# Optimization experiments

Hardware: AMD Instinct MI355X
Metric: run time of the kernel (lower is better)

The kernel has to match this reference:

```python
import jax, jax.numpy as jnp
import numpy as np
from jax import lax

CS = 64  # c_star


def _conv(x, w, pad, dil=1, groups=1):
    return lax.conv_general_dilated(
        x, w, (1, 1), ((pad[0], pad[0]), (pad[1], pad[1])),
        rhs_dilation=(dil, dil), dimension_numbers=('NCHW', 'OIHW', 'NCHW'),
        feature_group_count=groups)


def _bn(x, p, eps=1e-5):
    # p: [4, C] = (gamma, beta, running_mean, running_var), eval-mode batchnorm
    g, b, m, v = p
    s = g * lax.rsqrt(v + eps)
    return x * s[None, :, None, None] + (b - m * s)[None, :, None, None]


def _grid_sample(im, grid):
    # bilinear, padding_mode='zeros', align_corners=True
    # im: [B,C,H,W], grid: [B,H,W,2] with (x, y) in [-1, 1]
    B, C, H, W = im.shape
    gx = (grid[..., 0] + 1.0) * 0.5 * (W - 1)
    gy = (grid[..., 1] + 1.0) * 0.5 * (H - 1)
    x0 = jnp.floor(gx)
    y0 = jnp.floor(gy)
    wx = gx - x0
    wy = gy - y0

    def corner(ix, iy, w):
        valid = (ix >= 0) & (ix <= W - 1) & (iy >= 0) & (iy <= H - 1)
        ixc = jnp.clip(ix, 0, W - 1).astype(jnp.int32)
        iyc = jnp.clip(iy, 0, H - 1).astype(jnp.int32)
        vals = jax.vmap(lambda a, yy, xx: a[:, yy, xx])(im, iyc, ixc)  # [B,C,H,W]
        return vals * (w * valid)[:, None]

    return (corner(x0, y0, (1 - wx) * (1 - wy)) + corner(x0 + 1, y0, wx * (1 - wy))
            + corner(x0, y0 + 1, (1 - wx) * wy) + corner(x0 + 1, y0 + 1, wx * wy))


def _forward(x, w_reduce, bn_reduce, dcn_off_w, dcn_off_b, dcn_dw_w, dcn_pw_w, bn_dcn,
             w_d2, bn_d2, w_d3, bn_d3, w_asym1, bn_asym1, w_asym2, bn_asym2,
             ctx_weight, bn_star, eca_w, sp_w, blend_weight, w_expand, bn_expand):
    silu = jax.nn.silu
    h = silu(_bn(_conv(x, w_reduce, (0, 0)), bn_reduce))
    hs, hb = h[:, :CS], h[:, CS:]
    B, _, H, W = hs.shape
    # --- LightweightDCNv2 ---
    om = _conv(hs, dcn_off_w, (1, 1)) + dcn_off_b[None, :, None, None]
    off_y, off_x = om[:, 0], om[:, 1]
    mask = jax.nn.sigmoid(om[:, 2:3])
    gy, gx = jnp.meshgrid(jnp.linspace(-1.0, 1.0, H), jnp.linspace(-1.0, 1.0, W), indexing='ij')
    grid = jnp.stack([gx[None] + off_x * (2.0 / W), gy[None] + off_y * (2.0 / H)], axis=-1)
    xd = _grid_sample(hs, grid) * mask
    dcn = silu(_bn(_conv(_conv(xd, dcn_dw_w, (1, 1), groups=CS), dcn_pw_w, (0, 0)), bn_dcn))
    # --- context branches (depthwise dilated + asymmetric) ---
    d2 = silu(_bn(_conv(hs, w_d2, (2, 2), dil=2, groups=CS), bn_d2))
    d3 = silu(_bn(_conv(hs, w_d3, (3, 3), dil=3, groups=CS), bn_d3))
    a1 = silu(_bn(_conv(hs, w_asym1, (0, 3), groups=CS), bn_asym1))
    asym = silu(_bn(_conv(a1, w_asym2, (3, 0), groups=CS), bn_asym2))
    wv = jax.nn.softmax(ctx_weight)
    ctx = wv[0] * d2 + wv[1] * d3 + wv[2] * asym
    star = _bn(dcn * ctx, bn_star)
    # --- DualAttentionGate ---
    ych = star.mean((2, 3))[:, None, :]  # [B,1,C]
    ych = lax.conv_general_dilated(ych, eca_w, (1,), ((2, 2),),
                                   dimension_numbers=('NCH', 'OIH', 'NCH'))
    ych = jax.nn.sigmoid(ych).reshape(B, CS, 1, 1)
    star = star * ych
    sp = jnp.concatenate([star.mean(1, keepdims=True), star.max(1, keepdims=True)], axis=1)
    star = star * jax.nn.sigmoid(_conv(sp, sp_w, (3, 3)))
    # --- blend + shuffle + expand + residual ---
    alpha = jax.nn.sigmoid(blend_weight)
    out = jnp.concatenate([star * alpha, hb * (1.0 - alpha)], axis=1)
    c = out.shape[1]
    out = out.reshape(B, 2, c // 2, H, W).transpose(0, 2, 1, 3, 4).reshape(B, c, H, W)
    out = silu(_bn(_conv(out, w_expand, (0, 0)), bn_expand))
    return out + x


def setup_inputs() -> dict:
    ks = iter(jax.random.split(jax.random.key(0), 64))

    def nrm(shape, s=0.05):
        return jax.random.normal(next(ks), shape, jnp.float32) * s

    def bnp(C):
        return jnp.stack([1.0 + nrm((C,), 0.1), nrm((C,), 0.1), nrm((C,), 0.1),
                          0.5 + jax.random.uniform(next(ks), (C,), jnp.float32)])

    C1, C_, CSTAR = 256, 128, 64
    return dict(
        x=jax.random.normal(next(ks), (16, C1, 80, 80), jnp.float32),
        w_reduce=nrm((C_, C1, 1, 1)),
        bn_reduce=bnp(C_),
        dcn_off_w=nrm((3, CSTAR, 3, 3), 0.01),
        dcn_off_b=nrm((3,), 0.01),
        dcn_dw_w=nrm((CSTAR, 1, 3, 3), 0.2),
        dcn_pw_w=nrm((CSTAR, CSTAR, 1, 1), 0.1),
        bn_dcn=bnp(CSTAR),
        w_d2=nrm((CSTAR, 1, 3, 3), 0.2),
        bn_d2=bnp(CSTAR),
        w_d3=nrm((CSTAR, 1, 3, 3), 0.2),
        bn_d3=bnp(CSTAR),
        w_asym1=nrm((CSTAR, 1, 1, 7), 0.2),
        bn_asym1=bnp(CSTAR),
        w_asym2=nrm((CSTAR, 1, 7, 1), 0.2),
        bn_asym2=bnp(CSTAR),
        ctx_weight=jnp.ones(3, jnp.float32) / 3.0,
        bn_star=bnp(CSTAR),
        eca_w=nrm((1, 1, 5), 0.3),
        sp_w=nrm((1, 2, 7, 7), 0.1),
        blend_weight=jnp.asarray(0.5, jnp.float32),
        w_expand=nrm((C1, C_, 1, 1)),
        bn_expand=bnp(C1),
    )


def reference(x, w_reduce, bn_reduce, dcn_off_w, dcn_off_b, dcn_dw_w, dcn_pw_w, bn_dcn,
              w_d2, bn_d2, w_d3, bn_d3, w_asym1, bn_asym1, w_asym2, bn_asym2,
              ctx_weight, bn_star, eca_w, sp_w, blend_weight, w_expand, bn_expand):
    return _forward(x, w_reduce, bn_reduce, dcn_off_w, dcn_off_b, dcn_dw_w, dcn_pw_w, bn_dcn,
                    w_d2, bn_d2, w_d3, bn_d3, w_asym1, bn_asym1, w_asym2, bn_asym2,
                    ctx_weight, bn_star, eca_w, sp_w, blend_weight, w_expand, bn_expand)
```

## Files before the change

### kernel.cpp

```cpp
#include <hip/hip_runtime.h>

#define HH 80
#define WW 80
#define HWN 6400
#define BN 16

typedef unsigned short ushortT;
typedef __attribute__((ext_vector_type(8))) short short8;
typedef __attribute__((ext_vector_type(4))) float f32x4;

static constexpr size_t BIGN = (size_t)BN * 64 * HWN;

__device__ __forceinline__ float sigf(float v)  { return 1.f / (1.f + __expf(-v)); }
__device__ __forceinline__ float siluf(float v) { return v * sigf(v); }
__device__ __forceinline__ float bnap(float v, const float* __restrict__ bn, int c, int C) {
  float s = bn[c] * rsqrtf(bn[3 * C + c] + 1e-5f);
  return v * s + (bn[C + c] - bn[2 * C + c] * s);
}
__device__ __forceinline__ ushortT f2bf(float f) {
  unsigned u = __float_as_uint(f);
  return (ushortT)((u + 0x7FFFu + ((u >> 16) & 1u)) >> 16);
}
__device__ __forceinline__ void gl_lds16(const void* g, void* l) {
  __builtin_amdgcn_global_load_lds(
      (const __attribute__((address_space(1))) unsigned int*)g,
      (__attribute__((address_space(3))) unsigned int*)l, 16, 0, 0);
}
__device__ __forceinline__ int bs_w(int p, int k2) {
  return p * 20 + ((((k2 >> 2) ^ ((p >> 3) & 3)) << 2) | (k2 & 3));
}
__device__ __forceinline__ int bs_r(int p, int q) {
  return p * 20 + (((q ^ ((p >> 3) & 3)) << 2));
}

__global__ __launch_bounds__(256) void k_cvtw(const float* __restrict__ wr,
    const float* __restrict__ we, const float* __restrict__ wp,
    ushortT* __restrict__ wrb, ushortT* __restrict__ web, ushortT* __restrict__ wpb) {
  int i = blockIdx.x * 256 + threadIdx.x;
  if (i < 32768) wrb[i] = f2bf(wr[i]);
  else if (i < 65536) web[i - 32768] = f2bf(we[i - 32768]);
  else if (i < 69632) wpb[i - 65536] = f2bf(wp[i - 65536]);
}

__global__ __launch_bounds__(256) void k_reduce_mfma(
    const float* __restrict__ x, const ushortT* __restrict__ Wb,
    const float* __restrict__ bn, float* __restrict__ hs, float* __restrict__ hb) {
  __shared__ ushortT As[128 * 32];
  __shared__ unsigned BsU[128 * 20];
  __shared__ float Ep[4 * 16 * 68];
  const int t = threadIdx.x;
  const int w = t >> 6, l = t & 63;
  const int p0 = blockIdx.x * 128;
  const int b = blockIdx.z;
  const int wm = (w >> 1) * 64, wn = (w & 1) * 64;
  f32x4 acc[4][4] = {};
  const float* xb = x + (size_t)b * 256 * HWN;
  const int srow = l >> 2, scol = (l & 3) * 8;
  for (int k0 = 0; k0 < 256; k0 += 32) {
    __syncthreads();
    gl_lds16(Wb + (size_t)((w * 2) * 16 + srow) * 256 + k0 + scol, &As[(w * 2) * 16 * 32]);
    gl_lds16(Wb + (size_t)((w * 2 + 1) * 16 + srow) * 256 + k0 + scol, &As[(w * 2 + 1) * 16 * 32]);
#pragma unroll
    for (int pass = 0; pass < 8; ++pass) {
      int idx = pass * 256 + t;
      int p_l = idx & 127, k2 = idx >> 7;
      int k = k0 + 2 * k2;
      float v0 = xb[(size_t)k * HWN + p0 + p_l];
      float v1 = xb[(size_t)(k + 1) * HWN + p0 + p_l];
      BsU[bs_w(p_l, k2)] = (unsigned)f2bf(v0) | ((unsigned)f2bf(v1) << 16);
    }
    __syncthreads();
    const int q = l >> 4, r16 = l & 15;
    short8 a[4], bv[4];
#pragma unroll
    for (int i = 0; i < 4; ++i)
      a[i] = *reinterpret_cast<const short8*>(&As[(wm + i * 16 + r16) * 32 + q * 8]);
#pragma unroll
    for (int j = 0; j < 4; ++j) {
      int row = wn + j * 16 + r16;
      bv[j] = *reinterpret_cast<const short8*>(&BsU[bs_r(row, q)]);
    }
#pragma unroll
    for (int i = 0; i < 4; ++i)
#pragma unroll
      for (int j = 0; j < 4; ++j)
        acc[i][j] = __builtin_amdgcn_mfma_f32_16x16x32_bf16(a[i], bv[j], acc[i][j], 0, 0, 0);
  }
  float* T = Ep + w * (16 * 68);
  const int col = l & 15, rowq = (l >> 4) * 4;
#pragma unroll
  for (int i = 0; i < 4; ++i) {
#pragma unroll
    for (int r = 0; r < 4; ++r)
#pragma unroll
      for (int j = 0; j < 4; ++j)
        T[(rowq + r) * 68 + j * 16 + col] = acc[i][j][r];
#pragma unroll
    for (int pass = 0; pass < 4; ++pass) {
      int row_l = pass * 4 + (l >> 4);
      const float4 v = *reinterpret_cast<const float4*>(&T[row_l * 68 + col * 4]);
      int c = wm + i * 16 + row_l;
      float s = bn[c] * rsqrtf(bn[384 + c] + 1e-5f);
      float tt = bn[128 + c] - bn[256 + c] * s;
      float4 o;
      o.x = siluf(v.x * s + tt);
      o.y = siluf(v.y * s + tt);
      o.z = siluf(v.z * s + tt);
      o.w = siluf(v.w * s + tt);
      float* dst = (c < 64 ? hs : hb) + ((size_t)b * 64 + (c & 63)) * HWN + p0 + wn + col * 4;
      *reinterpret_cast<float4*>(dst) = o;
    }
  }
}

__global__ __launch_bounds__(256) void k_offset(const float* __restrict__ hs,
    const float* __restrict__ w, const float* __restrict__ bias,
    float* __restrict__ sx, float* __restrict__ sy, float* __restrict__ msk) {
  __shared__ float ht[16 * 324];
  __shared__ float wt[1728];
  const int t = threadIdx.x;
  const int b = blockIdx.y;
  const int x0 = (blockIdx.x % 5) * 16, y0 = (blockIdx.x / 5) * 16;
  const int lx = t & 15, ly = t >> 4;
  for (int i = t; i < 1728; i += 256) wt[i] = w[i];
  float a0 = 0.f, a1 = 0.f, a2 = 0.f;
  for (int r = 0; r < 4; ++r) {
    __syncthreads();
    for (int i = t; i < 16 * 324; i += 256) {
      int ch = i / 324, pos = i - ch * 324;
      int iy = pos / 18, ix = pos - iy * 18;
      int gy = y0 + iy - 1, gx = x0 + ix - 1;
      ht[i] = ((unsigned)gy < (unsigned)HH && (unsigned)gx < (unsigned)WW)
                  ? hs[((size_t)b * 64 + r * 16 + ch) * HWN + gy * WW + gx] : 0.f;
    }
    __syncthreads();
    for (int ch = 0; ch < 16; ++ch) {
      const float* base = &ht[ch * 324];
      const int c = r * 16 + ch;
#pragma unroll
      for (int dy = 0; dy < 3; ++dy)
#pragma unroll
        for (int dx = 0; dx < 3; ++dx) {
          float v = base[(ly + dy) * 18 + lx + dx];
          a0 = fmaf(wt[c * 9 + dy * 3 + dx], v, a0);
          a1 = fmaf(wt[576 + c * 9 + dy * 3 + dx], v, a1);
          a2 = fmaf(wt[1152 + c * 9 + dy * 3 + dx], v, a2);
        }
    }
  }
  a0 += bias[0];
  a1 += bias[1];
  a2 += bias[2];
  size_t o = (size_t)b * HWN + (y0 + ly) * WW + x0 + lx;
  const float sc = 79.f / 80.f;
  sx[o] = (float)(x0 + lx) + a1 * sc;
  sy[o] = (float)(y0 + ly) + a0 * sc;
  msk[o] = sigf(a2);
}

__global__ __launch_bounds__(256) void k_gsdw(const float* __restrict__ hs,
    const float* __restrict__ sx, const float* __restrict__ sy,
    const float* __restrict__ msk, const float* __restrict__ wdw,
    float* __restrict__ outp) {
  __shared__ float tile[18 * 18];
  const int t = threadIdx.x;
  const int c = blockIdx.y, b = blockIdx.z;
  const int tx0 = (blockIdx.x % 5) * 16, ty0 = (blockIdx.x / 5) * 16;
  const float* pl = hs + ((size_t)b * 64 + c) * HWN;
  for (int i = t; i < 324; i += 256) {
    int iy = i / 18, ix = i - iy * 18;
    int gy = ty0 + iy - 1, gx = tx0 + ix - 1;
    float v = 0.f;
    if ((unsigned)gy < (unsigned)HH && (unsigned)gx < (unsigned)WW) {
      size_t o = (size_t)b * HWN + gy * WW + gx;
      float gxs = sx[o], gys = sy[o], m = msk[o];
      float x0f = floorf(gxs), y0f = floorf(gys);
      float wx = gxs - x0f, wy = gys - y0f;
      int ix0 = (int)x0f, iy0 = (int)y0f;
      int ix1 = ix0 + 1, iy1 = iy0 + 1;
      float acc = 0.f;
      if ((unsigned)iy0 < (unsigned)HH && (unsigned)ix0 < (unsigned)WW) acc = fmaf(pl[iy0 * WW + ix0], (1.f - wx) * (1.f - wy), acc);
      if ((unsigned)iy0 < (unsigned)HH && (unsigned)ix1 < (unsigned)WW) acc = fmaf(pl[iy0 * WW + ix1], wx * (1.f - wy), acc);
      if ((unsigned)iy1 < (unsigned)HH && (unsigned)ix0 < (unsigned)WW) acc = fmaf(pl[iy1 * WW + ix0], (1.f - wx) * wy, acc);
      if ((unsigned)iy1 < (unsigned)HH && (unsigned)ix1 < (unsigned)WW) acc = fmaf(pl[iy1 * WW + ix1], wx * wy, acc);
      v = acc * m;
    }
    tile[i] = v;
  }
  __syncthreads();
  const int lx = t & 15, ly = t >> 4;
  const float* wc = wdw + c * 9;
  float acc = 0.f;
#pragma unroll
  for (int dy = 0; dy < 3; ++dy)
#pragma unroll
    for (int dx = 0; dx < 3; ++dx)
      acc = fmaf(wc[dy * 3 + dx], tile[(ly + dy) * 18 + lx + dx], acc);
  outp[((size_t)b * 64 + c) * HWN + (ty0 + ly) * WW + tx0 + lx] = acc;
}

__global__ __launch_bounds__(256) void k_pw_mfma(const float* __restrict__ in,
    const ushortT* __restrict__ Wpb, const float* __restrict__ bn,
    float* __restrict__ outp) {
  __shared__ ushortT As[2][64 * 32];
  __shared__ unsigned BsU[128 * 20];
  __shared__ float Ep[4 * 16 * 36];
  const int t = threadIdx.x;
  const int w = t >> 6, l = t & 63;
  const int p0 = blockIdx.x * 128;
  const int b = blockIdx.y;
  const int wn = w * 32;
  f32x4 acc[4][2] = {};
  const int srow = l >> 2, scol = (l & 3) * 8;
  gl_lds16(Wpb + (size_t)(w * 16 + srow) * 64 + scol,      &As[0][w * 16 * 32]);
  gl_lds16(Wpb + (size_t)(w * 16 + srow) * 64 + 32 + scol, &As[1][w * 16 * 32]);
  for (int kc = 0; kc < 2; ++kc) {
    __syncthreads();
    const int ch0 = kc * 32;
#pragma unroll
    for (int pass = 0; pass < 8; ++pass) {
      int idx = pass * 256 + t;
      int p_l = idx & 127, k2 = idx >> 7;
      int k = ch0 + 2 * k2;
      float v0 = in[((size_t)b * 64 + k) * HWN + p0 + p_l];
      float v1 = in[((size_t)b * 64 + k + 1) * HWN + p0 + p_l];
      BsU[bs_w(p_l, k2)] = (unsigned)f2bf(v0) | ((unsigned)f2bf(v1) << 16);
    }
    __syncthreads();
    const int q = l >> 4, r16 = l & 15;
    short8 a[4], bv[2];
#pragma unroll
    for (int i = 0; i < 4; ++i)
      a[i] = *reinterpret_cast<const short8*>(&As[kc][(i * 16 + r16) * 32 + q * 8]);
#pragma unroll
    for (int j = 0; j < 2; ++j)
      bv[j] = *reinterpret_cast<const short8*>(&BsU[bs_r(wn + j * 16 + r16, q)]);
#pragma unroll
    for (int i = 0; i < 4; ++i)
#pragma unroll
      for (int j = 0; j < 2; ++j)
        acc[i][j] = __builtin_amdgcn_mfma_f32_16x16x32_bf16(a[i], bv[j], acc[i][j], 0, 0, 0);
  }
  float* T = Ep + w * (16 * 36);
  const int col = l & 15, rowq = (l >> 4) * 4;
#pragma unroll
  for (int i = 0; i < 4; ++i) {
#pragma unroll
    for (int r = 0; r < 4; ++r)
#pragma unroll
      for (int j = 0; j < 2; ++j)
        T[(rowq + r) * 36 + j * 16 + col] = acc[i][j][r];
#pragma unroll
    for (int pass = 0; pass < 2; ++pass) {
      int flat = pass * 64 + l;
      int row_l = flat >> 3, c4 = flat & 7;
      const float4 v = *reinterpret_cast<const float4*>(&T[row_l * 36 + c4 * 4]);
      int c = i * 16 + row_l;
      float s = bn[c] * rsqrtf(bn[192 + c] + 1e-5f);
      float tt = bn[64 + c] - bn[128 + c] * s;
      float4 o;
      o.x = siluf(v.x * s + tt);
      o.y = siluf(v.y * s + tt);
      o.z = siluf(v.z * s + tt);
      o.w = siluf(v.w * s + tt);
      *reinterpret_cast<float4*>(outp + ((size_t)b * 64 + c) * HWN + p0 + wn + c4 * 4) = o;
    }
  }
}

__global__ __launch_bounds__(256) void k_ctxstar(const float* __restrict__ hs,
    const float* __restrict__ dcn,
    const float* __restrict__ wd2, const float* __restrict__ bnd2,
    const float* __restrict__ wd3, const float* __restrict__ bnd3,
    const float* __restrict__ wa1, const float* __restrict__ bna1,
    const float* __restrict__ wa2, const float* __restrict__ bna2,
    const float* __restrict__ cw, const float* __restrict__ bnstar,
    float* __restrict__ star0) {
  __shared__ float ht[22 * 23];
  __shared__ float at[22 * 17];
  const int t = threadIdx.x;
  const int c = blockIdx.y, b = blockIdx.z;
  const int tx0 = (blockIdx.x % 5) * 16, ty0 = (blockIdx.x / 5) * 16;
  const float* pl = hs + ((size_t)b * 64 + c) * HWN;
  for (int i = t; i < 484; i += 256) {
    int iy = i / 22, ix = i - iy * 22;
    int gy = ty0 + iy - 3, gx = tx0 + ix - 3;
    ht[iy * 23 + ix] = ((unsigned)gy < (unsigned)HH && (unsigned)gx < (unsigned)WW)
                           ? pl[gy * WW + gx] : 0.f;
  }
  __syncthreads();
  for (int i = t; i < 352; i += 256) {
    int iy = i >> 4, ix = i & 15;
    int gy = ty0 + iy - 3;
    float v = 0.f;
    if ((unsigned)gy < (unsigned)HH) {
      float s = 0.f;
#pragma unroll
      for (int k = 0; k < 7; ++k) s = fmaf(wa1[c * 7 + k], ht[iy * 23 + ix + k], s);
      v = siluf(bnap(s, bna1, c, 64));
    }
    at[iy * 17 + ix] = v;
  }
  __syncthreads();
  const int lx = t & 15, ly = t >> 4;
  float d2 = 0.f, d3 = 0.f;
#pragma unroll
  for (int dy = 0; dy < 3; ++dy)
#pragma unroll
    for (int dx = 0; dx < 3; ++dx) {
      float w2 = wd2[c * 9 + dy * 3 + dx], w3 = wd3[c * 9 + dy * 3 + dx];
      d2 = fmaf(w2, ht[(ly + 3 + 2 * (dy - 1)) * 23 + lx + 3 + 2 * (dx - 1)], d2);
      d3 = fmaf(w3, ht[(ly + 3 + 3 * (dy - 1)) * 23 + lx + 3 + 3 * (dx - 1)], d3);
    }
  float as = 0.f;
#pragma unroll
  for (int k = 0; k < 7; ++k) as = fmaf(wa2[c * 7 + k], at[(ly + k) * 17 + lx], as);
  d2 = siluf(bnap(d2, bnd2, c, 64));
  d3 = siluf(bnap(d3, bnd3, c, 64));
  as = siluf(bnap(as, bna2, c, 64));
  float e0 = __expf(cw[0]), e1 = __expf(cw[1]), e2 = __expf(cw[2]);
  float inv = 1.f / (e0 + e1 + e2);
  float ctx = (e0 * d2 + e1 * d3 + e2 * as) * inv;
  size_t o = ((size_t)b * 64 + c) * HWN + (ty0 + ly) * WW + tx0 + lx;
  star0[o] = bnap(dcn[o] * ctx, bnstar, c, 64);
}

__global__ __launch_bounds__(256) void k_cmean(const float* __restrict__ star0,
    float* __restrict__ mean) {
  const int c = blockIdx.x, b = blockIdx.y;
  const float* pl = star0 + ((size_t)b * 64 + c) * HWN;
  float s = 0.f;
  for (int i = threadIdx.x; i < HWN; i += 256) s += pl[i];
  __shared__ float red[256];
  red[threadIdx.x] = s;
  __syncthreads();
  for (int st = 128; st > 0; st >>= 1) {
    if (threadIdx.x < st) red[threadIdx.x] += red[threadIdx.x + st];
    __syncthreads();
  }
  if (threadIdx.x == 0) mean[b * 64 + c] = red[0] * (1.f / HWN);
}

__global__ __launch_bounds__(1024) void k_eca(const float* __restrict__ mean,
    const float* __restrict__ ew, float* __restrict__ ych) {
  const int t = threadIdx.x;
  const int c = t & 63;
  const int base = t - c;
  float acc = 0.f;
#pragma unroll
  for (int k = 0; k < 5; ++k) {
    int cc = c + k - 2;
    if ((unsigned)cc < 64u) acc = fmaf(ew[k], mean[base + cc], acc);
  }
  ych[t] = sigf(acc);
}

__global__ __launch_bounds__(256) void k_spstats(const float* __restrict__ star0,
    const float* __restrict__ ych, float* __restrict__ spmean, float* __restrict__ spmax) {
  __shared__ float yc[64];
  __shared__ float rs[4][64], rm[4][64];
  const int t = threadIdx.x;
  const int b = blockIdx.y;
  const int p0 = blockIdx.x * 64;
  if (t < 64) yc[t] = ych[b * 64 + t];
  __syncthreads();
  const int tq = t >> 6, pix = t & 63;
  float s = 0.f, mx = -1e30f;
  for (int cc = 0; cc < 16; ++cc) {
    int c = tq * 16 + cc;
    float v = star0[((size_t)b * 64 + c) * HWN + p0 + pix] * yc[c];
    s += v;
    mx = fmaxf(mx, v);
  }
  rs[tq][pix] = s;
  rm[tq][pix] = mx;
  __syncthreads();
  if (t < 64) {
    float ss = rs[0][t] + rs[1][t] + rs[2][t] + rs[3][t];
    float mm = fmaxf(fmaxf(rm[0][t], rm[1][t]), fmaxf(rm[2][t], rm[3][t]));
    spmean[(size_t)b * HWN + p0 + t] = ss * (1.f / 64.f);
    spmax[(size_t)b * HWN + p0 + t] = mm;
  }
}

__global__ __launch_bounds__(256) void k_spconv(const float* __restrict__ spmean,
    const float* __restrict__ spmax, const float* __restrict__ w,
    float* __restrict__ spat) {
  const int p = blockIdx.x * 256 + threadIdx.x;
  const int b = blockIdx.y;
  const int y = p / WW, x = p - y * WW;
  const float* me = spmean + (size_t)b * HWN;
  const float* mx = spmax + (size_t)b * HWN;
  float acc = 0.f;
#pragma unroll
  for (int dy = 0; dy < 7; ++dy) {
    int yy = y + dy - 3;
    if ((unsigned)yy >= (unsigned)HH) continue;
#pragma unroll
    for (int dx = 0; dx < 7; ++dx) {
      int xx = x + dx - 3;
      if ((unsigned)xx >= (unsigned)WW) continue;
      acc = fmaf(w[dy * 7 + dx], me[yy * WW + xx], acc);
      acc = fmaf(w[49 + dy * 7 + dx], mx[yy * WW + xx], acc);
    }
  }
  spat[(size_t)b * HWN + p] = sigf(acc);
}

__global__ __launch_bounds__(256) void k_expand_mfma(
    const float* __restrict__ star0, const float* __restrict__ hbuf,
    const float* __restrict__ ych, const float* __restrict__ spat,
    const float* __restrict__ blend, const ushortT* __restrict__ Wb,
    const float* __restrict__ bn, const float* __restrict__ xin,
    float* __restrict__ outp) {
  __shared__ ushortT As[128 * 32];
  __shared__ unsigned BsU[128 * 20];
  __shared__ float Ep[4 * 16 * 68];
  __shared__ float Sp[128];
  __shared__ float Yc[64];
  const int t = threadIdx.x;
  const int w = t >> 6, l = t & 63;
  const int p0 = blockIdx.x * 128;
  const int c0 = blockIdx.y * 128;
  const int b = blockIdx.z;
  const int wm = (w >> 1) * 64, wn = (w & 1) * 64;
  const float alpha = sigf(blend[0]);
  const float beta = 1.f - alpha;
  if (t < 128) Sp[t] = alpha * spat[(size_t)b * HWN + p0 + t];
  else if (t < 192) Yc[t - 128] = ych[b * 64 + (t - 128)];
  f32x4 acc[4][4] = {};
  const int srow = l >> 2, scol = (l & 3) * 8;
  for (int k0 = 0; k0 < 128; k0 += 32) {
    __syncthreads();
    gl_lds16(Wb + (size_t)(c0 + (w * 2) * 16 + srow) * 128 + k0 + scol, &As[(w * 2) * 16 * 32]);
    gl_lds16(Wb + (size_t)(c0 + (w * 2 + 1) * 16 + srow) * 128 + k0 + scol, &As[(w * 2 + 1) * 16 * 32]);
    const int ch0 = k0 >> 1;
#pragma unroll
    for (int pass = 0; pass < 8; ++pass) {
      int idx = pass * 256 + t;
      int p_l = idx & 127, chl = idx >> 7;
      int ch = ch0 + chl;
      size_t o = ((size_t)b * 64 + ch) * HWN + p0 + p_l;
      float vs = star0[o] * Yc[ch] * Sp[p_l];
      float vh = beta * hbuf[o];
      BsU[bs_w(p_l, chl)] = (unsigned)f2bf(vs) | ((unsigned)f2bf(vh) << 16);
    }
    __syncthreads();
    const int q = l >> 4, r16 = l & 15;
    short8 a[4], bv[4];
#pragma unroll
    for (int i = 0; i < 4; ++i)
      a[i] = *reinterpret_cast<const short8*>(&As[(wm + i * 16 + r16) * 32 + q * 8]);
#pragma unroll
    for (int j = 0; j < 4; ++j) {
      int row = wn + j * 16 + r16;
      bv[j] = *reinterpret_cast<const short8*>(&BsU[bs_r(row, q)]);
    }
#pragma unroll
    for (int i = 0; i < 4; ++i)
#pragma unroll
      for (int j = 0; j < 4; ++j)
        acc[i][j] = __builtin_amdgcn_mfma_f32_16x16x32_bf16(a[i], bv[j], acc[i][j], 0, 0, 0);
  }
  float* T = Ep + w * (16 * 68);
  const int col = l & 15, rowq = (l >> 4) * 4;
#pragma unroll
  for (int i = 0; i < 4; ++i) {
#pragma unroll
    for (int r = 0; r < 4; ++r)
#pragma unroll
      for (int j = 0; j < 4; ++j)
        T[(rowq + r) * 68 + j * 16 + col] = acc[i][j][r];
#pragma unroll
    for (int pass = 0; pass < 4; ++pass) {
      int row_l = pass * 4 + (l >> 4);
      const float4 v = *reinterpret_cast<const float4*>(&T[row_l * 68 + col * 4]);
      int c = c0 + wm + i * 16 + row_l;
      float s = bn[c] * rsqrtf(bn[768 + c] + 1e-5f);
      float tt = bn[256 + c] - bn[512 + c] * s;
      size_t o = ((size_t)b * 256 + c) * HWN + p0 + wn + col * 4;
      const float4 xr = *reinterpret_cast<const float4*>(xin + o);
      float4 ov;
      ov.x = siluf(v.x * s + tt) + xr.x;
      ov.y = siluf(v.y * s + tt) + xr.y;
      ov.z = siluf(v.z * s + tt) + xr.z;
      ov.w = siluf(v.w * s + tt) + xr.w;
      *reinterpret_cast<float4*>(outp + o) = ov;
    }
  }
}

extern "C" void kernel_launch(void* const* d_in, const int* in_sizes, int n_in,
                              void* d_out, int out_size, void* d_ws, size_t ws_size,
                              hipStream_t stream) {
  const float* x         = (const float*)d_in[0];
  const float* w_reduce  = (const float*)d_in[1];
  const float* bn_reduce = (const float*)d_in[2];
  const float* dcn_off_w = (const float*)d_in[3];
  const float* dcn_off_b = (const float*)d_in[4];
  const float* dcn_dw_w  = (const float*)d_in[5];
  const float* dcn_pw_w  = (const float*)d_in[6];
  const float* bn_dcn    = (const float*)d_in[7];
  const float* w_d2      = (const float*)d_in[8];
  const float* bn_d2     = (const float*)d_in[9];
  const float* w_d3      = (const float*)d_in[10];
  const float* bn_d3     = (const float*)d_in[11];
  const float* w_asym1   = (const float*)d_in[12];
  const float* bn_asym1  = (const float*)d_in[13];
  const float* w_asym2   = (const float*)d_in[14];
  const float* bn_asym2  = (const float*)d_in[15];
  const float* ctx_w     = (const float*)d_in[16];
  const float* bn_star   = (const float*)d_in[17];
  const float* eca_w     = (const float*)d_in[18];
  const float* sp_w      = (const float*)d_in[19];
  const float* blend     = (const float*)d_in[20];
  const float* w_expand  = (const float*)d_in[21];
  const float* bn_expand = (const float*)d_in[22];
  float* out = (float*)d_out;
  float* ws = (float*)d_ws;

  float* slotA = ws;
  float* slotB = ws + BIGN;
  float* slotC = ws + 2 * BIGN;
  float* slotD = ws + 3 * BIGN;
  float* sm = ws + 4 * BIGN;
  float* sx     = sm;
  float* sy     = sm + 102400;
  float* msk    = sm + 204800;
  float* spmean = sx;
  float* spmax  = sy;
  float* spat   = msk;
  float* cmean  = sm + 307200;
  float* ych    = sm + 308224;
  ushortT* Wrb = (ushortT*)(sm + 309248);
  ushortT* Web = Wrb + 32768;
  ushortT* Wpb = Web + 32768;

  k_cvtw<<<dim3(272), 256, 0, stream>>>(w_reduce, w_expand, dcn_pw_w, Wrb, Web, Wpb);
  k_reduce_mfma<<<dim3(50, 1, 16), 256, 0, stream>>>(x, Wrb, bn_reduce, slotA, slotB);
  k_offset<<<dim3(25, 16), 256, 0, stream>>>(slotA, dcn_off_w, dcn_off_b, sx, sy, msk);
  k_gsdw<<<dim3(25, 64, 16), 256, 0, stream>>>(slotA, sx, sy, msk, dcn_dw_w, slotC);
  k_pw_mfma<<<dim3(50, 16), 256, 0, stream>>>(slotC, Wpb, bn_dcn, slotD);
  k_ctxstar<<<dim3(25, 64, 16), 256, 0, stream>>>(slotA, slotD, w_d2, bn_d2,
                                                  w_d3, bn_d3, w_asym1, bn_asym1,
                                                  w_asym2, bn_asym2, ctx_w, bn_star, slotD);
  k_cmean<<<dim3(64, 16), 256, 0, stream>>>(slotD, cmean);
  k_eca<<<dim3(1), 1024, 0, stream>>>(cmean, eca_w, ych);
  k_spstats<<<dim3(100, 16), 256, 0, stream>>>(slotD, ych, spmean, spmax);
  k_spconv<<<dim3(25, 16), 256, 0, stream>>>(spmean, spmax, sp_w, spat);
  k_expand_mfma<<<dim3(50, 2, 16), 256, 0, stream>>>(slotD, slotB, ych, spat, blend,
                                                     Web, bn_expand, x, out);
}
```

Before: 478.1 us.

## Fuse channel-mean reduction into ctxstar epilogue and alias LDS buffers in MFMA kernels

```diff
diff --git a/kernel.cpp b/kernel.cpp
--- a/kernel.cpp
+++ b/kernel.cpp
@@ -35,19 +35,22 @@
 
 __global__ __launch_bounds__(256) void k_cvtw(const float* __restrict__ wr,
     const float* __restrict__ we, const float* __restrict__ wp,
-    ushortT* __restrict__ wrb, ushortT* __restrict__ web, ushortT* __restrict__ wpb) {
+    ushortT* __restrict__ wrb, ushortT* __restrict__ web, ushortT* __restrict__ wpb,
+    float* __restrict__ cmean) {
   int i = blockIdx.x * 256 + threadIdx.x;
   if (i < 32768) wrb[i] = f2bf(wr[i]);
   else if (i < 65536) web[i - 32768] = f2bf(we[i - 32768]);
   else if (i < 69632) wpb[i - 65536] = f2bf(wp[i - 65536]);
+  if (i < 1024) cmean[i] = 0.f;
 }
 
 __global__ __launch_bounds__(256) void k_reduce_mfma(
     const float* __restrict__ x, const ushortT* __restrict__ Wb,
     const float* __restrict__ bn, float* __restrict__ hs, float* __restrict__ hb) {
-  __shared__ ushortT As[128 * 32];
-  __shared__ unsigned BsU[128 * 20];
-  __shared__ float Ep[4 * 16 * 68];
+  __shared__ union {
+    struct { ushortT As[128 * 32]; unsigned BsU[128 * 20]; } s;
+    float Ep[4 * 16 * 68];
+  } sm;
   const int t = threadIdx.x;
   const int w = t >> 6, l = t & 63;
   const int p0 = blockIdx.x * 128;
@@ -58,8 +61,8 @@
   const int srow = l >> 2, scol = (l & 3) * 8;
   for (int k0 = 0; k0 < 256; k0 += 32) {
     __syncthreads();
-    gl_lds16(Wb + (size_t)((w * 2) * 16 + srow) * 256 + k0 + scol, &As[(w * 2) * 16 * 32]);
-    gl_lds16(Wb + (size_t)((w * 2 + 1) * 16 + srow) * 256 + k0 + scol, &As[(w * 2 + 1) * 16 * 32]);
+    gl_lds16(Wb + (size_t)((w * 2) * 16 + srow) * 256 + k0 + scol, &sm.s.As[(w * 2) * 16 * 32]);
+    gl_lds16(Wb + (size_t)((w * 2 + 1) * 16 + srow) * 256 + k0 + scol, &sm.s.As[(w * 2 + 1) * 16 * 32]);
 #pragma unroll
     for (int pass = 0; pass < 8; ++pass) {
       int idx = pass * 256 + t;
@@ -67,18 +70,18 @@
       int k = k0 + 2 * k2;
       float v0 = xb[(size_t)k * HWN + p0 + p_l];
       float v1 = xb[(size_t)(k + 1) * HWN + p0 + p_l];
-      BsU[bs_w(p_l, k2)] = (unsigned)f2bf(v0) | ((unsigned)f2bf(v1) << 16);
+      sm.s.BsU[bs_w(p_l, k2)] = (unsigned)f2bf(v0) | ((unsigned)f2bf(v1) << 16);
     }
     __syncthreads();
     const int q = l >> 4, r16 = l & 15;
     short8 a[4], bv[4];
 #pragma unroll
     for (int i = 0; i < 4; ++i)
-      a[i] = *reinterpret_cast<const short8*>(&As[(wm + i * 16 + r16) * 32 + q * 8]);
+      a[i] = *reinterpret_cast<const short8*>(&sm.s.As[(wm + i * 16 + r16) * 32 + q * 8]);
 #pragma unroll
     for (int j = 0; j < 4; ++j) {
       int row = wn + j * 16 + r16;
-      bv[j] = *reinterpret_cast<const short8*>(&BsU[bs_r(row, q)]);
+      bv[j] = *reinterpret_cast<const short8*>(&sm.s.BsU[bs_r(row, q)]);
     }
 #pragma unroll
     for (int i = 0; i < 4; ++i)
@@ -86,7 +89,8 @@
       for (int j = 0; j < 4; ++j)
         acc[i][j] = __builtin_amdgcn_mfma_f32_16x16x32_bf16(a[i], bv[j], acc[i][j], 0, 0, 0);
   }
-  float* T = Ep + w * (16 * 68);
+  __syncthreads();
+  float* T = sm.Ep + w * (16 * 68);
   const int col = l & 15, rowq = (l >> 4) * 4;
 #pragma unroll
   for (int i = 0; i < 4; ++i) {
@@ -202,9 +206,10 @@
 __global__ __launch_bounds__(256) void k_pw_mfma(const float* __restrict__ in,
     const ushortT* __restrict__ Wpb, const float* __restrict__ bn,
     float* __restrict__ outp) {
-  __shared__ ushortT As[2][64 * 32];
-  __shared__ unsigned BsU[128 * 20];
-  __shared__ float Ep[4 * 16 * 36];
+  __shared__ union {
+    struct { ushortT As[2][64 * 32]; unsigned BsU[128 * 20]; } s;
+    float Ep[4 * 16 * 36];
+  } sm;
   const int t = threadIdx.x;
   const int w = t >> 6, l = t & 63;
   const int p0 = blockIdx.x * 128;
@@ -212,8 +217,8 @@
   const int wn = w * 32;
   f32x4 acc[4][2] = {};
   const int srow = l >> 2, scol = (l & 3) * 8;
-  gl_lds16(Wpb + (size_t)(w * 16 + srow) * 64 + scol,      &As[0][w * 16 * 32]);
-  gl_lds16(Wpb + (size_t)(w * 16 + srow) * 64 + 32 + scol, &As[1][w * 16 * 32]);
+  gl_lds16(Wpb + (size_t)(w * 16 + srow) * 64 + scol,      &sm.s.As[0][w * 16 * 32]);
+  gl_lds16(Wpb + (size_t)(w * 16 + srow) * 64 + 32 + scol, &sm.s.As[1][w * 16 * 32]);
   for (int kc = 0; kc < 2; ++kc) {
     __syncthreads();
     const int ch0 = kc * 32;
@@ -224,24 +229,25 @@
       int k = ch0 + 2 * k2;
       float v0 = in[((size_t)b * 64 + k) * HWN + p0 + p_l];
       float v1 = in[((size_t)b * 64 + k + 1) * HWN + p0 + p_l];
-      BsU[bs_w(p_l, k2)] = (unsigned)f2bf(v0) | ((unsigned)f2bf(v1) << 16);
+      sm.s.BsU[bs_w(p_l, k2)] = (unsigned)f2bf(v0) | ((unsigned)f2bf(v1) << 16);
     }
     __syncthreads();
     const int q = l >> 4, r16 = l & 15;
     short8 a[4], bv[2];
 #pragma unroll
     for (int i = 0; i < 4; ++i)
-      a[i] = *reinterpret_cast<const short8*>(&As[kc][(i * 16 + r16) * 32 + q * 8]);
+      a[i] = *reinterpret_cast<const short8*>(&sm.s.As[kc][(i * 16 + r16) * 32 + q * 8]);
 #pragma unroll
     for (int j = 0; j < 2; ++j)
-      bv[j] = *reinterpret_cast<const short8*>(&BsU[bs_r(wn + j * 16 + r16, q)]);
+      bv[j] = *reinterpret_cast<const short8*>(&sm.s.BsU[bs_r(wn + j * 16 + r16, q)]);
 #pragma unroll
     for (int i = 0; i < 4; ++i)
 #pragma unroll
       for (int j = 0; j < 2; ++j)
         acc[i][j] = __builtin_amdgcn_mfma_f32_16x16x32_bf16(a[i], bv[j], acc[i][j], 0, 0, 0);
   }
-  float* T = Ep + w * (16 * 36);
+  __syncthreads();
+  float* T = sm.Ep + w * (16 * 36);
   const int col = l & 15, rowq = (l >> 4) * 4;
 #pragma unroll
   for (int i = 0; i < 4; ++i) {
@@ -275,7 +281,7 @@
     const float* __restrict__ wa1, const float* __restrict__ bna1,
     const float* __restrict__ wa2, const float* __restrict__ bna2,
     const float* __restrict__ cw, const float* __restrict__ bnstar,
-    float* __restrict__ star0) {
+    float* __restrict__ star0, float* __restrict__ cmean) {
   __shared__ float ht[22 * 23];
   __shared__ float at[22 * 17];
   const int t = threadIdx.x;
@@ -322,23 +328,16 @@
   float inv = 1.f / (e0 + e1 + e2);
   float ctx = (e0 * d2 + e1 * d3 + e2 * as) * inv;
   size_t o = ((size_t)b * 64 + c) * HWN + (ty0 + ly) * WW + tx0 + lx;
-  star0[o] = bnap(dcn[o] * ctx, bnstar, c, 64);
-}
-
-__global__ __launch_bounds__(256) void k_cmean(const float* __restrict__ star0,
-    float* __restrict__ mean) {
-  const int c = blockIdx.x, b = blockIdx.y;
-  const float* pl = star0 + ((size_t)b * 64 + c) * HWN;
-  float s = 0.f;
-  for (int i = threadIdx.x; i < HWN; i += 256) s += pl[i];
-  __shared__ float red[256];
-  red[threadIdx.x] = s;
+  float sv = bnap(dcn[o] * ctx, bnstar, c, 64);
+  star0[o] = sv;
+  __syncthreads();
+  ht[t] = sv;
   __syncthreads();
   for (int st = 128; st > 0; st >>= 1) {
-    if (threadIdx.x < st) red[threadIdx.x] += red[threadIdx.x + st];
-    __syncthreads();
-  }
-  if (threadIdx.x == 0) mean[b * 64 + c] = red[0] * (1.f / HWN);
+    if (t < st) ht[t] += ht[t + st];
+    __syncthreads();
+  }
+  if (t == 0) atomicAdd(&cmean[b * 64 + c], ht[0]);
 }
 
 __global__ __launch_bounds__(1024) void k_eca(const float* __restrict__ mean,
@@ -350,7 +349,7 @@
 #pragma unroll
   for (int k = 0; k < 5; ++k) {
     int cc = c + k - 2;
-    if ((unsigned)cc < 64u) acc = fmaf(ew[k], mean[base + cc], acc);
+    if ((unsigned)cc < 64u) acc = fmaf(ew[k], mean[base + cc] * (1.f / HWN), acc);
   }
   ych[t] = sigf(acc);
 }
@@ -413,9 +412,10 @@
     const float* __restrict__ blend, const ushortT* __restrict__ Wb,
     const float* __restrict__ bn, const float* __restrict__ xin,
     float* __restrict__ outp) {
-  __shared__ ushortT As[128 * 32];
-  __shared__ unsigned BsU[128 * 20];
-  __shared__ float Ep[4 * 16 * 68];
+  __shared__ union {
+    struct { ushortT As[128 * 32]; unsigned BsU[128 * 20]; } s;
+    float Ep[4 * 16 * 68];
+  } sm;
   __shared__ float Sp[128];
   __shared__ float Yc[64];
   const int t = threadIdx.x;
@@ -432,8 +432,8 @@
   const int srow = l >> 2, scol = (l & 3) * 8;
   for (int k0 = 0; k0 < 128; k0 += 32) {
     __syncthreads();
-    gl_lds16(Wb + (size_t)(c0 + (w * 2) * 16 + srow) * 128 + k0 + scol, &As[(w * 2) * 16 * 32]);
-    gl_lds16(Wb + (size_t)(c0 + (w * 2 + 1) * 16 + srow) * 128 + k0 + scol, &As[(w * 2 + 1) * 16 * 32]);
+    gl_lds16(Wb + (size_t)(c0 + (w * 2) * 16 + srow) * 128 + k0 + scol, &sm.s.As[(w * 2) * 16 * 32]);
+    gl_lds16(Wb + (size_t)(c0 + (w * 2 + 1) * 16 + srow) * 128 + k0 + scol, &sm.s.As[(w * 2 + 1) * 16 * 32]);
     const int ch0 = k0 >> 1;
 #pragma unroll
     for (int pass = 0; pass < 8; ++pass) {
@@ -443,18 +443,18 @@
       size_t o = ((size_t)b * 64 + ch) * HWN + p0 + p_l;
       float vs = star0[o] * Yc[ch] * Sp[p_l];
       float vh = beta * hbuf[o];
-      BsU[bs_w(p_l, chl)] = (unsigned)f2bf(vs) | ((unsigned)f2bf(vh) << 16);
+      sm.s.BsU[bs_w(p_l, chl)] = (unsigned)f2bf(vs) | ((unsigned)f2bf(vh) << 16);
     }
     __syncthreads();
     const int q = l >> 4, r16 = l & 15;
     short8 a[4], bv[4];
 #pragma unroll
     for (int i = 0; i < 4; ++i)
-      a[i] = *reinterpret_cast<const short8*>(&As[(wm + i * 16 + r16) * 32 + q * 8]);
+      a[i] = *reinterpret_cast<const short8*>(&sm.s.As[(wm + i * 16 + r16) * 32 + q * 8]);
 #pragma unroll
     for (int j = 0; j < 4; ++j) {
       int row = wn + j * 16 + r16;
-      bv[j] = *reinterpret_cast<const short8*>(&BsU[bs_r(row, q)]);
+      bv[j] = *reinterpret_cast<const short8*>(&sm.s.BsU[bs_r(row, q)]);
     }
 #pragma unroll
     for (int i = 0; i < 4; ++i)
@@ -462,7 +462,8 @@
       for (int j = 0; j < 4; ++j)
         acc[i][j] = __builtin_amdgcn_mfma_f32_16x16x32_bf16(a[i], bv[j], acc[i][j], 0, 0, 0);
   }
-  float* T = Ep + w * (16 * 68);
+  __syncthreads();
+  float* T = sm.Ep + w * (16 * 68);
   const int col = l & 15, rowq = (l >> 4) * 4;
 #pragma unroll
   for (int i = 0; i < 4; ++i) {
@@ -536,15 +537,15 @@
   ushortT* Web = Wrb + 32768;
   ushortT* Wpb = Web + 32768;
 
-  k_cvtw<<<dim3(272), 256, 0, stream>>>(w_reduce, w_expand, dcn_pw_w, Wrb, Web, Wpb);
+  k_cvtw<<<dim3(272), 256, 0, stream>>>(w_reduce, w_expand, dcn_pw_w, Wrb, Web, Wpb, cmean);
   k_reduce_mfma<<<dim3(50, 1, 16), 256, 0, stream>>>(x, Wrb, bn_reduce, slotA, slotB);
   k_offset<<<dim3(25, 16), 256, 0, stream>>>(slotA, dcn_off_w, dcn_off_b, sx, sy, msk);
   k_gsdw<<<dim3(25, 64, 16), 256, 0, stream>>>(slotA, sx, sy, msk, dcn_dw_w, slotC);
   k_pw_mfma<<<dim3(50, 16), 256, 0, stream>>>(slotC, Wpb, bn_dcn, slotD);
   k_ctxstar<<<dim3(25, 64, 16), 256, 0, stream>>>(slotA, slotD, w_d2, bn_d2,
                                                   w_d3, bn_d3, w_asym1, bn_asym1,
-                                                  w_asym2, bn_asym2, ctx_w, bn_star, slotD);
-  k_cmean<<<dim3(64, 16), 256, 0, stream>>>(slotD, cmean);
+                                                  w_asym2, bn_asym2, ctx_w, bn_star,
+                                                  slotD, cmean);
   k_eca<<<dim3(1), 1024, 0, stream>>>(cmean, eca_w, ych);
   k_spstats<<<dim3(100, 16), 256, 0, stream>>>(slotD, ych, spmean, spmax);
   k_spconv<<<dim3(25, 16), 256, 0, stream>>>(spmean, spmax, sp_w, spat);
```

After: 517.9 us. +8.3%, slower.
